# Performance work log

Hardware: AMD Instinct MI355X
Metric: run time of the kernel (lower is better)

## Reference

```python
import jax, jax.numpy as jnp
import numpy as np

# plane_axes buffer from the torch module (permutation matrices)
PLANE_AXES = jnp.array([[[0, 1, 0], [1, 0, 0], [0, 0, 1]],
                        [[0, 0, 1], [1, 0, 0], [0, 1, 0]],
                        [[0, 1, 0], [0, 0, 1], [1, 0, 0]]], dtype=jnp.float32)

M = 1_000_000
C = 32
R = 512


def setup_inputs() -> dict:
    key = jax.random.key(0)
    k1, k2 = jax.random.split(key)
    # query points uniform in [-1, 1]^3 (grid_sample coordinate convention)
    xyz = jax.random.uniform(k1, (M, 3), dtype=jnp.float32) * 2.0 - 1.0
    triplane = jax.random.normal(k2, (1, 3, C, R, R), dtype=jnp.float32) * 0.05
    return {"xyz": xyz, "triplane": triplane, "oid": 0}


def _grid_sample_plane(img, gx, gy):
    """Bilinear grid_sample, align_corners=True, padding_mode='zeros'.
    img: [C, H, W]; gx, gy: [M] normalized coords in [-1, 1] (x -> W, y -> H).
    Returns [C, M]."""
    _, H, W = img.shape
    x = (gx + 1.0) * 0.5 * (W - 1)  # align_corners=True unnormalization
    y = (gy + 1.0) * 0.5 * (H - 1)
    x0 = jnp.floor(x)
    y0 = jnp.floor(y)
    x1 = x0 + 1.0
    y1 = y0 + 1.0
    wx1 = x - x0
    wx0 = 1.0 - wx1
    wy1 = y - y0
    wy0 = 1.0 - wy1

    def corner(xi, yi, w):
        valid = (xi >= 0) & (xi <= W - 1) & (yi >= 0) & (yi <= H - 1)
        xi_c = jnp.clip(xi, 0, W - 1).astype(jnp.int32)
        yi_c = jnp.clip(yi, 0, H - 1).astype(jnp.int32)
        vals = img[:, yi_c, xi_c]  # [C, M] gather
        return vals * (w * valid)[None, :]

    return (corner(x0, y0, wx0 * wy0) + corner(x1, y0, wx1 * wy0)
            + corner(x0, y1, wx0 * wy1) + corner(x1, y1, wx1 * wy1))


def reference(xyz, triplane, oid):
    # project_onto_planes: xyz [M,3] -> projections [3, M, 2]
    inv_planes = jnp.linalg.inv(PLANE_AXES)           # [3, 3, 3]
    proj = jnp.einsum('mk,pkj->pmj', xyz, inv_planes)[..., :2]  # [3, M, 2]
    planes = triplane[oid]                            # [3, C, R, R]
    # grid coords: last dim is (x, y) per torch grid_sample convention
    sampled = jax.vmap(_grid_sample_plane)(planes, proj[..., 0], proj[..., 1])  # [3, C, M]
    # permute(0,3,2,1).reshape(3,M,C).sum(0) -> [M, C]
    return sampled.sum(0).T
```

## Files before the change

kernel.cpp:

```cpp
#include <hip/hip_runtime.h>
#include <hip/hip_bf16.h>


#define RRTP 262144
#define CTP  32
#define NB   512
#define SORT_P 4096
#define TPBLK 3072
#define PLANE_B (RRTP * 64)

typedef float        f32x4 __attribute__((ext_vector_type(4)));
typedef unsigned int u32;
typedef u32          u32x4 __attribute__((ext_vector_type(4)));

__device__ __forceinline__ u32 part3b(u32 v) {
    return (v & 1) | ((v & 2) << 2) | ((v & 4) << 4);
}
__device__ __forceinline__ u32 morton9(float px, float py, float pz) {
    int qx = max(0, min(7, (int)((px + 1.0f) * 4.0f)));
    int qy = max(0, min(7, (int)((py + 1.0f) * 4.0f)));
    int qz = max(0, min(7, (int)((pz + 1.0f) * 4.0f)));
    return part3b((u32)qx) | (part3b((u32)qy) << 1) | (part3b((u32)qz) << 2);
}

__global__ __launch_bounds__(256) void tp_fused(const float* __restrict__ in,
                                                u32* __restrict__ texels,
                                                const float* __restrict__ xyz,
                                                u32* __restrict__ hist,
                                                const int* __restrict__ oid, int Mtot) {
    __shared__ float tile[256][33];
    const int t = threadIdx.x;

    if (blockIdx.x < TPBLK) {
        const int b     = blockIdx.x;
        const int plane = b >> 10;
        const int rr0   = (b & 1023) << 8;

        const float* src = in + (size_t)oid[0] * (3u * CTP * RRTP)
                              + (size_t)plane * (CTP * RRTP) + rr0 + t;
        #pragma unroll
        for (int c = 0; c < 32; ++c)
            tile[t][c] = src[(size_t)c * RRTP];
        __syncthreads();

        u32* dst = texels + (size_t)plane * ((size_t)RRTP * 16) + (size_t)rr0 * 16;
        const int cp = t & 15;
        #pragma unroll
        for (int k = 0; k < 16; ++k) {
            const int r = (k << 4) + (t >> 4);
            const float f0 = tile[r][cp * 2];
            const float f1 = tile[r][cp * 2 + 1];
            const u32 lo = (u32)__bfloat16_as_ushort(__float2bfloat16(f0));
            const u32 hi = (u32)__bfloat16_as_ushort(__float2bfloat16(f1));
            dst[(size_t)r * 16 + cp] = (hi << 16) | lo;
        }
    } else {
        u32* cnt = (u32*)&tile[0][0];
        const int b = blockIdx.x - TPBLK;
        cnt[t] = 0u; cnt[t + 256] = 0u;
        __syncthreads();
        const int base_m = b * SORT_P;
        #pragma unroll
        for (int i = 0; i < 16; ++i) {
            const int m = base_m + i * 256 + t;
            if (m < Mtot) {
                const u32 k = morton9(xyz[3 * m], xyz[3 * m + 1], xyz[3 * m + 2]);
                atomicAdd(&cnt[k], 1u);
            }
        }
        __syncthreads();
        hist[b * NB + t] = cnt[t];
        hist[b * NB + t + 256] = cnt[t + 256];
    }
}

__global__ __launch_bounds__(512) void tp_scanB(u32* __restrict__ hist,
                                                u32* __restrict__ bucket_base, int nblk) {
    const int k = threadIdx.x;
    u32 run = 0;
    #pragma unroll 8
    for (int b = 0; b < nblk; ++b) {
        const u32 v = hist[b * NB + k];
        hist[b * NB + k] = run;
        run += v;
    }
    __shared__ u32 sA[NB], sB[NB];
    sA[k] = run;
    int par = 0;
    for (int off = 1; off < NB; off <<= 1) {
        __syncthreads();
        u32* src = par ? sB : sA;
        u32* dst = par ? sA : sB;
        dst[k] = src[k] + ((k >= off) ? src[k - off] : 0u);
        par ^= 1;
    }
    __syncthreads();
    const u32 incl = (par ? sB : sA)[k];
    bucket_base[k] = incl - run;
}

__global__ __launch_bounds__(256) void tp_scatter_blk(const float* __restrict__ xyz,
                                                      const u32* __restrict__ hist,
                                                      const u32* __restrict__ bucket_base,
                                                      f32x4* __restrict__ sorted, int Mtot) {
    __shared__ u32 goff[NB];
    __shared__ u32 sA[NB], sB[NB];
    __shared__ f32x4 rec[SORT_P];
    __shared__ unsigned short lkey[SORT_P];
    const int t = threadIdx.x, b = blockIdx.x;
    const int base_m = b * SORT_P;

    sA[t] = 0u; sA[t + 256] = 0u;
    goff[t]       = bucket_base[t]       + hist[b * NB + t];
    goff[t + 256] = bucket_base[t + 256] + hist[b * NB + t + 256];
    __syncthreads();

    float xs[16], ys[16], zs[16]; u32 ks[16], rs[16];
    #pragma unroll
    for (int i = 0; i < 16; ++i) {
        const int m = base_m + i * 256 + t;
        const bool v = (m < Mtot);
        float px = 0.f, py = 0.f, pz = 0.f;
        if (v) { px = xyz[3 * m]; py = xyz[3 * m + 1]; pz = xyz[3 * m + 2]; }
        const u32 key = morton9(px, py, pz);
        xs[i] = px; ys[i] = py; zs[i] = pz;
        ks[i] = v ? key : 0xffffffffu;
        rs[i] = v ? atomicAdd(&sA[key], 1u) : 0u;
    }
    __syncthreads();

    const u32 c0 = sA[t], c1 = sA[t + 256];
    int par = 0;
    for (int off = 1; off < NB; off <<= 1) {
        u32* src = par ? sB : sA;
        u32* dst = par ? sA : sB;
        const u32 a0 = src[t]       + ((t >= off)       ? src[t - off]       : 0u);
        const u32 a1 = src[t + 256] + ((t + 256 >= off) ? src[t + 256 - off] : 0u);
        dst[t] = a0; dst[t + 256] = a1;
        par ^= 1;
        __syncthreads();
    }
    u32* incl = par ? sB : sA;
    const u32 lb0 = incl[t] - c0, lb1 = incl[t + 256] - c1;
    __syncthreads();
    sA[t] = lb0; sA[t + 256] = lb1;
    goff[t] -= lb0; goff[t + 256] -= lb1;
    __syncthreads();

    #pragma unroll
    for (int i = 0; i < 16; ++i) {
        if (ks[i] != 0xffffffffu) {
            const u32 pos = sA[ks[i]] + rs[i];
            f32x4 r = {xs[i], ys[i], zs[i],
                       __uint_as_float((u32)(base_m + i * 256 + t))};
            rec[pos] = r;
            lkey[pos] = (unsigned short)ks[i];
        }
    }
    __syncthreads();

    const int nv = min(SORT_P, Mtot - base_m);
    #pragma unroll
    for (int i = 0; i < 16; ++i) {
        const int s = i * 256 + t;
        if (s < nv) {
            const u32 k2 = lkey[s];
            sorted[goff[k2] + s] = rec[s];
        }
    }
}

__global__ __launch_bounds__(256) void tp_sample_sorted(const f32x4* __restrict__ sorted,
                                                        const u32* __restrict__ tp,
                                                        float* __restrict__ out,
                                                        int Mtot, int nwg) {
    const int bid = blockIdx.x;
    const int qc = nwg >> 3, rc = nwg & 7;
    const int xcd = bid & 7, j = bid >> 3;
    const int wg = ((xcd < rc) ? xcd * (qc + 1) : rc * (qc + 1) + (xcd - rc) * qc) + j;

    const int tid = wg * 256 + threadIdx.x;
    const int sp = tid >> 2;
    if (sp >= Mtot) return;
    const u32 oq = (u32)((tid & 3) << 4);

    const f32x4 pt = sorted[sp];
    const float px = pt.x, py = pt.y, pz = pt.z;
    const u32 m = __float_as_uint(pt.w);

    const float gxs[3] = {py, pz, py};
    const float gys[3] = {px, px, pz};

    f32x4 alo = {0.f, 0.f, 0.f, 0.f};
    f32x4 ahi = {0.f, 0.f, 0.f, 0.f};

    const char* tpc = (const char*)tp;

    #pragma unroll
    for (int p = 0; p < 3; ++p) {
        const float xf = (gxs[p] + 1.0f) * (0.5f * 511.0f);
        const float yf = (gys[p] + 1.0f) * (0.5f * 511.0f);
        const float x0f = floorf(xf), y0f = floorf(yf);
        float wx1 = xf - x0f, wy1 = yf - y0f;
        float wx0 = 1.0f - wx1, wy0 = 1.0f - wy1;

        int x0 = (int)x0f, y0 = (int)y0f;
        int x1 = x0 + 1,   y1 = y0 + 1;
        if (x1 > 511) { x1 = 511; wx1 = 0.0f; }
        if (y1 > 511) { y1 = 511; wy1 = 0.0f; }
        x0 = max(0, min(511, x0));
        y0 = max(0, min(511, y0));

        const u32 ry0 = ((u32)y0 << 15), ry1 = ((u32)y1 << 15);
        const u32 cx0 = ((u32)x0 << 6)  + oq, cx1 = ((u32)x1 << 6) + oq;
        const char* base_p = tpc + (size_t)p * PLANE_B;

        const u32x4 v00 = *(const u32x4*)(base_p + (ry0 + cx0));
        const u32x4 v01 = *(const u32x4*)(base_p + (ry0 + cx1));
        const u32x4 v10 = *(const u32x4*)(base_p + (ry1 + cx0));
        const u32x4 v11 = *(const u32x4*)(base_p + (ry1 + cx1));

        const float w00 = wy0 * wx0, w01 = wy0 * wx1;
        const float w10 = wy1 * wx0, w11 = wy1 * wx1;

        #pragma unroll
        for (int i = 0; i < 4; ++i) {
            const float l00 = __uint_as_float(v00[i] << 16), h00 = __uint_as_float(v00[i] & 0xffff0000u);
            const float l01 = __uint_as_float(v01[i] << 16), h01 = __uint_as_float(v01[i] & 0xffff0000u);
            const float l10 = __uint_as_float(v10[i] << 16), h10 = __uint_as_float(v10[i] & 0xffff0000u);
            const float l11 = __uint_as_float(v11[i] << 16), h11 = __uint_as_float(v11[i] & 0xffff0000u);
            alo[i] = fmaf(w00, l00, fmaf(w01, l01, fmaf(w10, l10, fmaf(w11, l11, alo[i]))));
            ahi[i] = fmaf(w00, h00, fmaf(w01, h01, fmaf(w10, h10, fmaf(w11, h11, ahi[i]))));
        }
    }

    float* ob = out + ((size_t)m << 5) + (size_t)(oq >> 1);
    f32x4 s0 = {alo[0], ahi[0], alo[1], ahi[1]};
    f32x4 s1 = {alo[2], ahi[2], alo[3], ahi[3]};
    __builtin_nontemporal_store(s0, (f32x4*)ob);
    __builtin_nontemporal_store(s1, (f32x4*)(ob + 4));
}

__global__ __launch_bounds__(256) void tp_sample_direct(const float* __restrict__ xyz,
                                                        const float* __restrict__ tpl,
                                                        const int* __restrict__ oid,
                                                        float* __restrict__ out,
                                                        int Mtot) {
    const int tid = blockIdx.x * 256 + threadIdx.x;
    const int m = tid >> 5;
    if (m >= Mtot) return;
    const int c = tid & 31;
    const float px = xyz[m * 3 + 0], py = xyz[m * 3 + 1], pz = xyz[m * 3 + 2];
    const float gxs[3] = {py, pz, py};
    const float gys[3] = {px, px, pz};
    const float* base = tpl + (size_t)oid[0] * (3u * CTP * RRTP);
    float acc = 0.f;
    #pragma unroll
    for (int p = 0; p < 3; ++p) {
        const float xf = (gxs[p] + 1.0f) * (0.5f * 511.0f);
        const float yf = (gys[p] + 1.0f) * (0.5f * 511.0f);
        const float x0f = floorf(xf), y0f = floorf(yf);
        float wx1 = xf - x0f, wy1 = yf - y0f;
        float wx0 = 1.0f - wx1, wy0 = 1.0f - wy1;
        int x0 = (int)x0f, y0 = (int)y0f;
        int x1 = x0 + 1,   y1 = y0 + 1;
        if (x1 > 511) { x1 = 511; wx1 = 0.0f; }
        if (y1 > 511) { y1 = 511; wy1 = 0.0f; }
        x0 = max(0, min(511, x0));
        y0 = max(0, min(511, y0));
        const float* img = base + ((size_t)p * CTP + c) * RRTP;
        acc += wy0 * (wx0 * img[(y0 << 9) + x0] + wx1 * img[(y0 << 9) + x1])
             + wy1 * (wx0 * img[(y1 << 9) + x0] + wx1 * img[(y1 << 9) + x1]);
    }
    out[((size_t)m << 5) + c] = acc;
}

extern "C" void kernel_launch(void* const* d_in, const int* in_sizes, int n_in,
                              void* d_out, int out_size, void* d_ws, size_t ws_size,
                              hipStream_t stream) {
    const float* xyz      = (const float*)d_in[0];
    const float* triplane = (const float*)d_in[1];
    const int*   oid      = (const int*)d_in[2];
    float*       out      = (float*)d_out;
    const int Mtot = in_sizes[0] / 3;
    const int nblk = (Mtot + SORT_P - 1) / SORT_P;

    const size_t hist_b   = 512 * 1024;
    const size_t bb_off   = hist_b;
    const size_t sorted_off = hist_b + 64 * 1024;
    const size_t sorted_b = (size_t)Mtot * 16;
    const size_t texel_off = sorted_off + sorted_b;
    const size_t texel_b  = (size_t)3 * RRTP * 16 * 4;
    const size_t ws_needed = texel_off + texel_b;

    if (ws_size >= ws_needed && (size_t)nblk * NB * 4 <= hist_b) {
        u32*   hist   = (u32*)d_ws;
        u32*   bbase  = (u32*)((char*)d_ws + bb_off);
        f32x4* sorted = (f32x4*)((char*)d_ws + sorted_off);
        u32*   texels = (u32*)((char*)d_ws + texel_off);

        tp_fused<<<TPBLK + nblk, 256, 0, stream>>>(triplane, texels, xyz, hist, oid, Mtot);
        tp_scanB<<<1, 512, 0, stream>>>(hist, bbase, nblk);
        tp_scatter_blk<<<nblk, 256, 0, stream>>>(xyz, hist, bbase, sorted, Mtot);

        const int nwg = (Mtot * 4 + 255) / 256;
        tp_sample_sorted<<<nwg, 256, 0, stream>>>(sorted, texels, out, Mtot, nwg);
    } else {
        tp_sample_direct<<<(Mtot * 32 + 255) / 256, 256, 0, stream>>>(xyz, triplane, oid, out, Mtot);
    }
}
```

Before: 135.6 us.

## Move triplane transpose into scatter kernel and split histogram into own launch

Moves the triplane fp32-to-bf16 texel transpose out of the histogram kernel and into the same launch as the point scatter, so the small histogram kernel runs alone before the scan. The larger scatter work now overlaps with the bandwidth-heavy transpose instead of the histogram doing so. In exchange, every block of the fused kernel reserves about 78KB of shared memory, including the transpose blocks that need only about 33KB. That can reduce how many transpose blocks fit on each CU at once.

```diff
diff --git a/kernel.cpp b/kernel.cpp
--- a/kernel.cpp
+++ b/kernel.cpp
@@ -23,55 +23,24 @@
     return part3b((u32)qx) | (part3b((u32)qy) << 1) | (part3b((u32)qz) << 2);
 }
 
-__global__ __launch_bounds__(256) void tp_fused(const float* __restrict__ in,
-                                                u32* __restrict__ texels,
-                                                const float* __restrict__ xyz,
-                                                u32* __restrict__ hist,
-                                                const int* __restrict__ oid, int Mtot) {
-    __shared__ float tile[256][33];
-    const int t = threadIdx.x;
-
-    if (blockIdx.x < TPBLK) {
-        const int b     = blockIdx.x;
-        const int plane = b >> 10;
-        const int rr0   = (b & 1023) << 8;
-
-        const float* src = in + (size_t)oid[0] * (3u * CTP * RRTP)
-                              + (size_t)plane * (CTP * RRTP) + rr0 + t;
-        #pragma unroll
-        for (int c = 0; c < 32; ++c)
-            tile[t][c] = src[(size_t)c * RRTP];
-        __syncthreads();
-
-        u32* dst = texels + (size_t)plane * ((size_t)RRTP * 16) + (size_t)rr0 * 16;
-        const int cp = t & 15;
-        #pragma unroll
-        for (int k = 0; k < 16; ++k) {
-            const int r = (k << 4) + (t >> 4);
-            const float f0 = tile[r][cp * 2];
-            const float f1 = tile[r][cp * 2 + 1];
-            const u32 lo = (u32)__bfloat16_as_ushort(__float2bfloat16(f0));
-            const u32 hi = (u32)__bfloat16_as_ushort(__float2bfloat16(f1));
-            dst[(size_t)r * 16 + cp] = (hi << 16) | lo;
-        }
-    } else {
-        u32* cnt = (u32*)&tile[0][0];
-        const int b = blockIdx.x - TPBLK;
-        cnt[t] = 0u; cnt[t + 256] = 0u;
-        __syncthreads();
-        const int base_m = b * SORT_P;
-        #pragma unroll
-        for (int i = 0; i < 16; ++i) {
-            const int m = base_m + i * 256 + t;
-            if (m < Mtot) {
-                const u32 k = morton9(xyz[3 * m], xyz[3 * m + 1], xyz[3 * m + 2]);
-                atomicAdd(&cnt[k], 1u);
-            }
-        }
-        __syncthreads();
-        hist[b * NB + t] = cnt[t];
-        hist[b * NB + t + 256] = cnt[t + 256];
-    }
+__global__ __launch_bounds__(256) void tp_hist_blk(const float* __restrict__ xyz,
+                                                   u32* __restrict__ hist, int Mtot) {
+    __shared__ u32 cnt[NB];
+    const int t = threadIdx.x, b = blockIdx.x;
+    cnt[t] = 0u; cnt[t + 256] = 0u;
+    __syncthreads();
+    const int base_m = b * SORT_P;
+    #pragma unroll
+    for (int i = 0; i < 16; ++i) {
+        const int m = base_m + i * 256 + t;
+        if (m < Mtot) {
+            const u32 k = morton9(xyz[3 * m], xyz[3 * m + 1], xyz[3 * m + 2]);
+            atomicAdd(&cnt[k], 1u);
+        }
+    }
+    __syncthreads();
+    hist[b * NB + t] = cnt[t];
+    hist[b * NB + t + 256] = cnt[t + 256];
 }
 
 __global__ __launch_bounds__(512) void tp_scanB(u32* __restrict__ hist,
@@ -99,73 +68,107 @@
     bucket_base[k] = incl - run;
 }
 
-__global__ __launch_bounds__(256) void tp_scatter_blk(const float* __restrict__ xyz,
-                                                      const u32* __restrict__ hist,
-                                                      const u32* __restrict__ bucket_base,
-                                                      f32x4* __restrict__ sorted, int Mtot) {
-    __shared__ u32 goff[NB];
-    __shared__ u32 sA[NB], sB[NB];
-    __shared__ f32x4 rec[SORT_P];
-    __shared__ unsigned short lkey[SORT_P];
-    const int t = threadIdx.x, b = blockIdx.x;
-    const int base_m = b * SORT_P;
-
-    sA[t] = 0u; sA[t + 256] = 0u;
-    goff[t]       = bucket_base[t]       + hist[b * NB + t];
-    goff[t + 256] = bucket_base[t + 256] + hist[b * NB + t + 256];
-    __syncthreads();
-
-    float xs[16], ys[16], zs[16]; u32 ks[16], rs[16];
-    #pragma unroll
-    for (int i = 0; i < 16; ++i) {
-        const int m = base_m + i * 256 + t;
-        const bool v = (m < Mtot);
-        float px = 0.f, py = 0.f, pz = 0.f;
-        if (v) { px = xyz[3 * m]; py = xyz[3 * m + 1]; pz = xyz[3 * m + 2]; }
-        const u32 key = morton9(px, py, pz);
-        xs[i] = px; ys[i] = py; zs[i] = pz;
-        ks[i] = v ? key : 0xffffffffu;
-        rs[i] = v ? atomicAdd(&sA[key], 1u) : 0u;
-    }
-    __syncthreads();
-
-    const u32 c0 = sA[t], c1 = sA[t + 256];
-    int par = 0;
-    for (int off = 1; off < NB; off <<= 1) {
-        u32* src = par ? sB : sA;
-        u32* dst = par ? sA : sB;
-        const u32 a0 = src[t]       + ((t >= off)       ? src[t - off]       : 0u);
-        const u32 a1 = src[t + 256] + ((t + 256 >= off) ? src[t + 256 - off] : 0u);
-        dst[t] = a0; dst[t + 256] = a1;
-        par ^= 1;
-        __syncthreads();
-    }
-    u32* incl = par ? sB : sA;
-    const u32 lb0 = incl[t] - c0, lb1 = incl[t + 256] - c1;
-    __syncthreads();
-    sA[t] = lb0; sA[t + 256] = lb1;
-    goff[t] -= lb0; goff[t + 256] -= lb1;
-    __syncthreads();
-
-    #pragma unroll
-    for (int i = 0; i < 16; ++i) {
-        if (ks[i] != 0xffffffffu) {
-            const u32 pos = sA[ks[i]] + rs[i];
-            f32x4 r = {xs[i], ys[i], zs[i],
-                       __uint_as_float((u32)(base_m + i * 256 + t))};
-            rec[pos] = r;
-            lkey[pos] = (unsigned short)ks[i];
-        }
-    }
-    __syncthreads();
-
-    const int nv = min(SORT_P, Mtot - base_m);
-    #pragma unroll
-    for (int i = 0; i < 16; ++i) {
-        const int s = i * 256 + t;
-        if (s < nv) {
-            const u32 k2 = lkey[s];
-            sorted[goff[k2] + s] = rec[s];
+__global__ __launch_bounds__(256) void tp_fused2(const float* __restrict__ in,
+                                                 u32* __restrict__ texels,
+                                                 const float* __restrict__ xyz,
+                                                 const u32* __restrict__ hist,
+                                                 const u32* __restrict__ bucket_base,
+                                                 f32x4* __restrict__ sorted,
+                                                 const int* __restrict__ oid, int Mtot) {
+    __shared__ alignas(16) char smem[79872];
+    const int t = threadIdx.x;
+
+    if (blockIdx.x < TPBLK) {
+        float (*tile)[33] = (float(*)[33])smem;
+        const int b     = blockIdx.x;
+        const int plane = b >> 10;
+        const int rr0   = (b & 1023) << 8;
+
+        const float* src = in + (size_t)oid[0] * (3u * CTP * RRTP)
+                              + (size_t)plane * (CTP * RRTP) + rr0 + t;
+        #pragma unroll
+        for (int c = 0; c < 32; ++c)
+            tile[t][c] = src[(size_t)c * RRTP];
+        __syncthreads();
+
+        u32* dst = texels + (size_t)plane * ((size_t)RRTP * 16) + (size_t)rr0 * 16;
+        const int cp = t & 15;
+        #pragma unroll
+        for (int k = 0; k < 16; ++k) {
+            const int r = (k << 4) + (t >> 4);
+            const float f0 = tile[r][cp * 2];
+            const float f1 = tile[r][cp * 2 + 1];
+            const u32 lo = (u32)__bfloat16_as_ushort(__float2bfloat16(f0));
+            const u32 hi = (u32)__bfloat16_as_ushort(__float2bfloat16(f1));
+            dst[(size_t)r * 16 + cp] = (hi << 16) | lo;
+        }
+    } else {
+        f32x4* rec = (f32x4*)smem;
+        u32*   goff = (u32*)(smem + 65536);
+        u32*   sA   = (u32*)(smem + 67584);
+        u32*   sB   = (u32*)(smem + 69632);
+        unsigned short* lkey = (unsigned short*)(smem + 71680);
+
+        const int b = blockIdx.x - TPBLK;
+        const int base_m = b * SORT_P;
+
+        sA[t] = 0u; sA[t + 256] = 0u;
+        goff[t]       = bucket_base[t]       + hist[b * NB + t];
+        goff[t + 256] = bucket_base[t + 256] + hist[b * NB + t + 256];
+        __syncthreads();
+
+        float xs[16], ys[16], zs[16]; u32 ks[16], rs[16];
+        #pragma unroll
+        for (int i = 0; i < 16; ++i) {
+            const int m = base_m + i * 256 + t;
+            const bool v = (m < Mtot);
+            float px = 0.f, py = 0.f, pz = 0.f;
+            if (v) { px = xyz[3 * m]; py = xyz[3 * m + 1]; pz = xyz[3 * m + 2]; }
+            const u32 key = morton9(px, py, pz);
+            xs[i] = px; ys[i] = py; zs[i] = pz;
+            ks[i] = v ? key : 0xffffffffu;
+            rs[i] = v ? atomicAdd(&sA[key], 1u) : 0u;
+        }
+        __syncthreads();
+
+        const u32 c0 = sA[t], c1 = sA[t + 256];
+        int par = 0;
+        for (int off = 1; off < NB; off <<= 1) {
+            u32* srcp = par ? sB : sA;
+            u32* dstp = par ? sA : sB;
+            const u32 a0 = srcp[t]       + ((t >= off)       ? srcp[t - off]       : 0u);
+            const u32 a1 = srcp[t + 256] + ((t + 256 >= off) ? srcp[t + 256 - off] : 0u);
+            dstp[t] = a0; dstp[t + 256] = a1;
+            par ^= 1;
+            __syncthreads();
+        }
+        u32* incl = par ? sB : sA;
+        const u32 lb0 = incl[t] - c0, lb1 = incl[t + 256] - c1;
+        __syncthreads();
+        sA[t] = lb0; sA[t + 256] = lb1;
+        goff[t] -= lb0; goff[t + 256] -= lb1;
+        __syncthreads();
+
+        #pragma unroll
+        for (int i = 0; i < 16; ++i) {
+            if (ks[i] != 0xffffffffu) {
+                const u32 pos = sA[ks[i]] + rs[i];
+                f32x4 r = {xs[i], ys[i], zs[i],
+                           __uint_as_float((u32)(base_m + i * 256 + t))};
+                rec[pos] = r;
+                lkey[pos] = (unsigned short)ks[i];
+            }
+        }
+        __syncthreads();
+
+        const int nv = min(SORT_P, Mtot - base_m);
+        #pragma unroll
+        for (int i = 0; i < 16; ++i) {
+            const int s = i * 256 + t;
+            if (s < nv) {
+                const u32 k2 = lkey[s];
+                sorted[goff[k2] + s] = rec[s];
+            }
         }
     }
 }
@@ -299,9 +302,10 @@
         f32x4* sorted = (f32x4*)((char*)d_ws + sorted_off);
         u32*   texels = (u32*)((char*)d_ws + texel_off);
 
-        tp_fused<<<TPBLK + nblk, 256, 0, stream>>>(triplane, texels, xyz, hist, oid, Mtot);
+        tp_hist_blk<<<nblk, 256, 0, stream>>>(xyz, hist, Mtot);
         tp_scanB<<<1, 512, 0, stream>>>(hist, bbase, nblk);
-        tp_scatter_blk<<<nblk, 256, 0, stream>>>(xyz, hist, bbase, sorted, Mtot);
+        tp_fused2<<<TPBLK + nblk, 256, 0, stream>>>(triplane, texels, xyz, hist,
+                                                    bbase, sorted, oid, Mtot);
 
         const int nwg = (Mtot * 4 + 255) / 256;
         tp_sample_sorted<<<nwg, 256, 0, stream>>>(sorted, texels, out, Mtot, nwg);
```

Measured after the change: 142.3 us. +4.9%, slower.
